# Performance work log

Hardware: AMD Instinct MI355X
Metric: run time of the kernel (lower is better)

The kernel has to match this reference:

```python
import jax, jax.numpy as jnp
import numpy as np

N = 8192
DIM_IN = 256
DIM_Q = 64
DIM_K = 64
E = 262144


def setup_inputs() -> dict:
    key = jax.random.key(0)
    ks = jax.random.split(key, 8)
    x = jax.random.normal(ks[0], (N, DIM_IN), dtype=jnp.float32)
    edge_index = jax.random.randint(ks[1], (2, E), 0, N, dtype=jnp.int64)
    s_in = 1.0 / np.sqrt(DIM_IN)
    Wq = jax.random.normal(ks[2], (DIM_IN, DIM_Q), dtype=jnp.float32) * s_in
    bq = jnp.zeros((DIM_Q,), dtype=jnp.float32)
    Wk = jax.random.normal(ks[3], (DIM_IN, DIM_K), dtype=jnp.float32) * s_in
    bk = jnp.zeros((DIM_K,), dtype=jnp.float32)
    Wv = jax.random.normal(ks[4], (DIM_IN, DIM_K), dtype=jnp.float32) * s_in
    bv = jnp.zeros((DIM_K,), dtype=jnp.float32)
    return {"x": x, "edge_index": edge_index, "Wq": Wq, "bq": bq,
            "Wk": Wk, "bk": bk, "Wv": Wv, "bv": bv}


def reference(x, edge_index, Wq, bq, Wk, bk, Wv, bv):
    # q/k/v projections (Dense layers)
    q = x @ Wq + bq            # (N, dim_q)
    k = x @ Wk + bk            # (N, dim_k)
    v = x @ Wv + bv            # (N, dim_k)
    n = x.shape[0]
    # scatter-built dense adjacency, as in the original module
    adj = jnp.zeros((n, n), dtype=x.dtype).at[edge_index[0], edge_index[1]].set(1.0)
    scale = 1.0 / jnp.sqrt(jnp.asarray(q.shape[-1], dtype=x.dtype))
    a = (q @ k.T) * scale      # (N, N)
    a = a * adj + (1.0 - adj) * (-1000000.0)
    attn = jax.nn.softmax(a, axis=-1)
    return attn @ v            # (N, dim_k)
```

## Files before the change

### kernel.cpp

```cpp
#include <hip/hip_runtime.h>
#include <hip/hip_bf16.h>

#define NROW 8192
#define DIM_IN 256
#define DIMK 64
#define NDIM 192
#define NEDGE 262144
#define BUCKET 128

using bf16 = __hip_bfloat16;
typedef _Float16 f16;
typedef _Float16 f16x8 __attribute__((ext_vector_type(8)));
typedef _Float16 f16x4 __attribute__((ext_vector_type(4)));
typedef float f32x4 __attribute__((ext_vector_type(4)));

__device__ __forceinline__ float b2f(bf16 x) { return __bfloat162float(x); }
__device__ __forceinline__ float us2f(unsigned short u) {
    return __uint_as_float(((unsigned)u) << 16);
}
__device__ __forceinline__ void wave_sync() {
    asm volatile("s_waitcnt lgkmcnt(0)" ::: "memory");
    __builtin_amdgcn_sched_barrier(0);
}

__global__ __launch_bounds__(256) void probe_kernel(
    const unsigned short* __restrict__ xw, const int* __restrict__ ei,
    int* __restrict__ cursor, int* __restrict__ eflag, int* __restrict__ fflag)
{
    int gid = blockIdx.x * 256 + threadIdx.x;
    cursor[gid] = 0;
    if (blockIdx.x == 0) {
        __shared__ int cnt, ebad;
        int t = threadIdx.x;
        if (t == 0) { cnt = 0; ebad = 0; }
        __syncthreads();
        if (t < 128) {
            int ex = (xw[t] >> 7) & 0xFF;
            if (ex >= 100 && ex <= 140) atomicAdd(&cnt, 1);
            if (t < 64 && ei[2 * t + 1] != 0) atomicAdd(&ebad, 1);
        }
        __syncthreads();
        if (t == 0) {
            *fflag = (cnt >= 110) ? 1 : 0;
            *eflag = (ebad == 0) ? 1 : 0;
        }
    }
}

__device__ __forceinline__ int src_at(const int* p, int e, int is64) {
    return is64 ? p[2 * e] : p[e];
}
__device__ __forceinline__ int dst_at(const int* p, int e, int is64) {
    return is64 ? p[2 * (NEDGE + e)] : p[NEDGE + e];
}

__global__ __launch_bounds__(256) void prep_kernel(
    const void* __restrict__ x,
    const void* __restrict__ Wq, const void* __restrict__ Wk,
    const void* __restrict__ Wv, const int* __restrict__ fflag,
    f16* __restrict__ xh, f16* __restrict__ wt)
{
    int isb = *fflag;
    int i = blockIdx.x * 256 + threadIdx.x;
    f16x4 o;
    if (isb) {
        ushort4 u = ((const ushort4*)x)[i];
        o.x = (f16)us2f(u.x); o.y = (f16)us2f(u.y);
        o.z = (f16)us2f(u.z); o.w = (f16)us2f(u.w);
    } else {
        float4 f = ((const float4*)x)[i];
        o.x = (f16)f.x; o.y = (f16)f.y; o.z = (f16)f.z; o.w = (f16)f.w;
    }
    *(f16x4*)(xh + 4 * i) = o;

    if (blockIdx.x < NDIM) {
        int d = blockIdx.x, c = threadIdx.x;
        int mat = d >> 6, dd = d & 63;
        const void* W = (mat == 0) ? Wq : (mat == 1) ? Wk : Wv;
        float val = isb ? b2f(((const bf16*)W)[c * DIMK + dd])
                        : ((const float*)W)[c * DIMK + dd];
        wt[d * DIM_IN + c] = (f16)val;
    }
}

__global__ __launch_bounds__(512) void proj_mfma_kernel(
    const f16* __restrict__ xh, const f16* __restrict__ wt,
    const void* __restrict__ bq, const void* __restrict__ bk,
    const void* __restrict__ bv, const int* __restrict__ fflag,
    f16* __restrict__ q, f16* __restrict__ k, f16* __restrict__ v)
{
    int t = threadIdx.x;
    int wave = t >> 6, lane = t & 63;
    int rowg = wave >> 2, colg = wave & 3;
    int r0 = blockIdx.x * 32 + rowg * 16;
    int n0 = colg * 48;
    int lr = lane & 15;
    int lk = (lane >> 4) * 8;

    f32x4 acc0 = {0.f, 0.f, 0.f, 0.f}, acc1 = acc0, acc2 = acc0;
    const f16* ap = xh + (size_t)(r0 + lr) * DIM_IN + lk;
    const f16* bp = wt + (size_t)(n0 + lr) * DIM_IN + lk;

    #pragma unroll
    for (int ks = 0; ks < 8; ++ks) {
        f16x8 a  = *(const f16x8*)(ap + ks * 32);
        f16x8 b0 = *(const f16x8*)(bp + ks * 32);
        f16x8 b1 = *(const f16x8*)(bp + 16 * DIM_IN + ks * 32);
        f16x8 b2 = *(const f16x8*)(bp + 32 * DIM_IN + ks * 32);
        acc0 = __builtin_amdgcn_mfma_f32_16x16x32_f16(a, b0, acc0, 0, 0, 0);
        acc1 = __builtin_amdgcn_mfma_f32_16x16x32_f16(a, b1, acc1, 0, 0, 0);
        acc2 = __builtin_amdgcn_mfma_f32_16x16x32_f16(a, b2, acc2, 0, 0, 0);
    }

    int isb = *fflag;
    #pragma unroll
    for (int tt = 0; tt < 3; ++tt) {
        f32x4 a = (tt == 0) ? acc0 : (tt == 1) ? acc1 : acc2;
        int d = n0 + tt * 16 + lr;
        int mat = d >> 6, dd = d & 63;
        const void* bb = (mat == 0) ? bq : (mat == 1) ? bk : bv;
        float bias = isb ? b2f(((const bf16*)bb)[dd]) : ((const float*)bb)[dd];
        f16* o = (mat == 0) ? q : (mat == 1) ? k : v;
        #pragma unroll
        for (int j = 0; j < 4; ++j) {
            int r = r0 + (lane >> 4) * 4 + j;
            o[(size_t)r * DIMK + dd] = (f16)(a[j] + bias);
        }
    }
}

__global__ __launch_bounds__(256) void scatter_kernel(
    const int* __restrict__ p, const int* __restrict__ eflag,
    int* __restrict__ cursor, unsigned short* __restrict__ colsbuf)
{
    int e = blockIdx.x * 256 + threadIdx.x;
    int is64 = *eflag;
    int r = src_at(p, e, is64);
    int c = dst_at(p, e, is64);
    int pos = atomicAdd(&cursor[r], 1);
    if (pos < BUCKET) colsbuf[(size_t)r * BUCKET + pos] = (unsigned short)c;
}

__global__ __launch_bounds__(256) void attn_kernel(
    const f16* __restrict__ q, const f16* __restrict__ k,
    const f16* __restrict__ v, const int* __restrict__ cursor,
    const unsigned short* __restrict__ colsbuf, float* __restrict__ out)
{
    __shared__ unsigned bm_all[4][NROW / 32];
    __shared__ unsigned short nb_all[4][BUCKET];
    __shared__ float sc_all[4][BUCKET];

    int t = threadIdx.x, wave = t >> 6, lane = t & 63;
    int row = blockIdx.x * 4 + wave;
    unsigned* bm = bm_all[wave];
    unsigned short* nb = nb_all[wave];
    float* sc = sc_all[wave];

    *(uint4*)(bm + 4 * lane) = make_uint4(0u, 0u, 0u, 0u);
    wave_sync();

    int deg = cursor[row];
    if (deg > BUCKET) deg = BUCKET;
    const unsigned short* bucket = colsbuf + (size_t)row * BUCKET;
    for (int e = lane; e < deg; e += 64) {
        int j = bucket[e];
        atomicOr(&bm[j >> 5], 1u << (j & 31));
    }
    wave_sync();

    uint4 wv = *(const uint4*)(bm + 4 * lane);
    int pc = __popc(wv.x) + __popc(wv.y) + __popc(wv.z) + __popc(wv.w);
    int incl = pc;
    #pragma unroll
    for (int o = 1; o < 64; o <<= 1) {
        int n = __shfl_up(incl, o);
        if (lane >= o) incl += n;
    }
    int nn = __shfl(incl, 63);
    int idx = incl - pc;
    unsigned wrds[4] = {wv.x, wv.y, wv.z, wv.w};
    #pragma unroll
    for (int wi = 0; wi < 4; ++wi) {
        unsigned wb = wrds[wi];
        int boff = 128 * lane + 32 * wi;
        while (wb) {
            int b = __ffs(wb) - 1;
            wb &= wb - 1;
            nb[idx++] = (unsigned short)(boff + b);
        }
    }
    wave_sync();

    if (nn == 0) {
        out[(size_t)row * DIMK + lane] = 0.f;
        return;
    }

    int g = lane >> 4, gl = lane & 15;
    f16x4 qh4 = *(const f16x4*)(q + (size_t)row * DIMK + 4 * gl);
    float q0 = (float)qh4.x, q1 = (float)qh4.y, q2 = (float)qh4.z, q3 = (float)qh4.w;
    for (int i = g; i < nn; i += 4) {
        int j = nb[i];
        f16x4 kk = *(const f16x4*)(k + (size_t)j * DIMK + 4 * gl);
        float d = q0 * (float)kk.x + q1 * (float)kk.y
                + q2 * (float)kk.z + q3 * (float)kk.w;
        #pragma unroll
        for (int o = 1; o < 16; o <<= 1) d += __shfl_xor(d, o);
        if (gl == 0) sc[i] = d * 0.125f;
    }
    wave_sync();

    float s0 = (lane < nn) ? sc[lane] : -INFINITY;
    float s1 = (lane + 64 < nn) ? sc[lane + 64] : -INFINITY;
    float mx = fmaxf(s0, s1);
    #pragma unroll
    for (int o = 1; o < 64; o <<= 1) mx = fmaxf(mx, __shfl_xor(mx, o));
    float w0 = (lane < nn) ? __expf(s0 - mx) : 0.f;
    float w1 = (lane + 64 < nn) ? __expf(s1 - mx) : 0.f;
    if (lane < nn) sc[lane] = w0;
    if (lane + 64 < nn) sc[lane + 64] = w1;
    float sm = w0 + w1;
    #pragma unroll
    for (int o = 1; o < 64; o <<= 1) sm += __shfl_xor(sm, o);
    wave_sync();

    float acc = 0.f;
    int i = 0;
    for (; i + 4 <= nn; i += 4) {
        int j0 = nb[i], j1 = nb[i + 1], j2 = nb[i + 2], j3 = nb[i + 3];
        float v0 = (float)v[(size_t)j0 * DIMK + lane];
        float v1 = (float)v[(size_t)j1 * DIMK + lane];
        float v2 = (float)v[(size_t)j2 * DIMK + lane];
        float v3 = (float)v[(size_t)j3 * DIMK + lane];
        acc = fmaf(sc[i], v0, acc);
        acc = fmaf(sc[i + 1], v1, acc);
        acc = fmaf(sc[i + 2], v2, acc);
        acc = fmaf(sc[i + 3], v3, acc);
    }
    for (; i < nn; ++i)
        acc = fmaf(sc[i], (float)v[(size_t)nb[i] * DIMK + lane], acc);

    out[(size_t)row * DIMK + lane] = acc / sm;
}

extern "C" void kernel_launch(void* const* d_in, const int* in_sizes, int n_in,
                              void* d_out, int out_size, void* d_ws, size_t ws_size,
                              hipStream_t stream)
{
    const void* x  = d_in[0];
    const int*  ei = (const int*)d_in[1];
    const void* Wq = d_in[2];
    const void* bq = d_in[3];
    const void* Wk = d_in[4];
    const void* bk = d_in[5];
    const void* Wv = d_in[6];
    const void* bv = d_in[7];
    float* out = (float*)d_out;

    char* W8 = (char*)d_ws;
    f16* xh = (f16*)W8;
    unsigned short* colsbuf = (unsigned short*)W8;
    f16* wt = (f16*)(W8 + (size_t)4 * 1024 * 1024);
    f16* qh = (f16*)(W8 + (size_t)4 * 1024 * 1024 + 98304);
    f16* kh = qh + (size_t)NROW * DIMK;
    f16* vh = kh + (size_t)NROW * DIMK;
    int* cursor = (int*)(vh + (size_t)NROW * DIMK);
    int* eflag = cursor + NROW;
    int* fflag = eflag + 1;
    size_t need = (size_t)((char*)(fflag + 1) - W8);
    if (ws_size < need) return;

    probe_kernel<<<32, 256, 0, stream>>>((const unsigned short*)x, ei,
                                         cursor, eflag, fflag);
    prep_kernel<<<2048, 256, 0, stream>>>(x, Wq, Wk, Wv, fflag, xh, wt);
    proj_mfma_kernel<<<NROW / 32, 512, 0, stream>>>(xh, wt, bq, bk, bv, fflag,
                                                    qh, kh, vh);
    scatter_kernel<<<NEDGE / 256, 256, 0, stream>>>(ei, eflag, cursor, colsbuf);
    attn_kernel<<<NROW / 4, 256, 0, stream>>>(qh, kh, vh, cursor, colsbuf, out);
}
```

Baseline: 52.67 us.

## Build global adjacency bitmap in projection kernel, drop probe and scatter kernels

```diff
diff --git a/kernel.cpp b/kernel.cpp
--- a/kernel.cpp
+++ b/kernel.cpp
@@ -6,7 +6,8 @@
 #define DIMK 64
 #define NDIM 192
 #define NEDGE 262144
-#define BUCKET 128
+#define NBW (NROW / 32)
+#define CAP 128
 
 using bf16 = __hip_bfloat16;
 typedef _Float16 f16;
@@ -23,30 +24,15 @@
     __builtin_amdgcn_sched_barrier(0);
 }
 
-__global__ __launch_bounds__(256) void probe_kernel(
-    const unsigned short* __restrict__ xw, const int* __restrict__ ei,
-    int* __restrict__ cursor, int* __restrict__ eflag, int* __restrict__ fflag)
-{
-    int gid = blockIdx.x * 256 + threadIdx.x;
-    cursor[gid] = 0;
-    if (blockIdx.x == 0) {
-        __shared__ int cnt, ebad;
-        int t = threadIdx.x;
-        if (t == 0) { cnt = 0; ebad = 0; }
-        __syncthreads();
-        if (t < 128) {
-            int ex = (xw[t] >> 7) & 0xFF;
-            if (ex >= 100 && ex <= 140) atomicAdd(&cnt, 1);
-            if (t < 64 && ei[2 * t + 1] != 0) atomicAdd(&ebad, 1);
-        }
-        __syncthreads();
-        if (t == 0) {
-            *fflag = (cnt >= 110) ? 1 : 0;
-            *eflag = (ebad == 0) ? 1 : 0;
-        }
-    }
-}
-
+__device__ __forceinline__ int probe_isb(const unsigned short* xw, int lane) {
+    int ex = (xw[lane] >> 7) & 0xFF;
+    unsigned long long b = __ballot(ex >= 100 && ex <= 140);
+    return (__popcll(b) >= 56) ? 1 : 0;
+}
+__device__ __forceinline__ int probe_is64(const int* ei, int lane) {
+    unsigned long long b = __ballot(ei[2 * lane + 1] != 0);
+    return (b == 0ULL) ? 1 : 0;
+}
 __device__ __forceinline__ int src_at(const int* p, int e, int is64) {
     return is64 ? p[2 * e] : p[e];
 }
@@ -57,11 +43,15 @@
 __global__ __launch_bounds__(256) void prep_kernel(
     const void* __restrict__ x,
     const void* __restrict__ Wq, const void* __restrict__ Wk,
-    const void* __restrict__ Wv, const int* __restrict__ fflag,
-    f16* __restrict__ xh, f16* __restrict__ wt)
-{
-    int isb = *fflag;
-    int i = blockIdx.x * 256 + threadIdx.x;
+    const void* __restrict__ Wv,
+    f16* __restrict__ xh, f16* __restrict__ wt, unsigned* __restrict__ gbm)
+{
+    int t = threadIdx.x, lane = t & 63;
+    int isb = probe_isb((const unsigned short*)x, lane);
+    int i = blockIdx.x * 256 + t;
+
+    ((uint4*)gbm)[i] = make_uint4(0u, 0u, 0u, 0u);
+
     f16x4 o;
     if (isb) {
         ushort4 u = ((const ushort4*)x)[i];
@@ -74,7 +64,7 @@
     *(f16x4*)(xh + 4 * i) = o;
 
     if (blockIdx.x < NDIM) {
-        int d = blockIdx.x, c = threadIdx.x;
+        int d = blockIdx.x, c = t;
         int mat = d >> 6, dd = d & 63;
         const void* W = (mat == 0) ? Wq : (mat == 1) ? Wk : Wv;
         float val = isb ? b2f(((const bf16*)W)[c * DIMK + dd])
@@ -83,14 +73,26 @@
     }
 }
 
-__global__ __launch_bounds__(512) void proj_mfma_kernel(
+__global__ __launch_bounds__(512) void proj_scatter_kernel(
     const f16* __restrict__ xh, const f16* __restrict__ wt,
     const void* __restrict__ bq, const void* __restrict__ bk,
-    const void* __restrict__ bv, const int* __restrict__ fflag,
+    const void* __restrict__ bv,
+    const unsigned short* __restrict__ xw, const int* __restrict__ ei,
+    unsigned* __restrict__ gbm,
     f16* __restrict__ q, f16* __restrict__ k, f16* __restrict__ v)
 {
     int t = threadIdx.x;
     int wave = t >> 6, lane = t & 63;
+
+    int is64 = probe_is64(ei, lane);
+    #pragma unroll
+    for (int ii = 0; ii < 2; ++ii) {
+        int e = blockIdx.x * 1024 + t + ii * 512;
+        int r = src_at(ei, e, is64) & (NROW - 1);
+        int c = dst_at(ei, e, is64) & (NROW - 1);
+        atomicOr(&gbm[r * NBW + (c >> 5)], 1u << (c & 31));
+    }
+
     int rowg = wave >> 2, colg = wave & 3;
     int r0 = blockIdx.x * 32 + rowg * 16;
     int n0 = colg * 48;
@@ -112,7 +114,7 @@
         acc2 = __builtin_amdgcn_mfma_f32_16x16x32_f16(a, b2, acc2, 0, 0, 0);
     }
 
-    int isb = *fflag;
+    int isb = probe_isb(xw, lane);
     #pragma unroll
     for (int tt = 0; tt < 3; ++tt) {
         f32x4 a = (tt == 0) ? acc0 : (tt == 1) ? acc1 : acc2;
@@ -129,46 +131,20 @@
     }
 }
 
-__global__ __launch_bounds__(256) void scatter_kernel(
-    const int* __restrict__ p, const int* __restrict__ eflag,
-    int* __restrict__ cursor, unsigned short* __restrict__ colsbuf)
-{
-    int e = blockIdx.x * 256 + threadIdx.x;
-    int is64 = *eflag;
-    int r = src_at(p, e, is64);
-    int c = dst_at(p, e, is64);
-    int pos = atomicAdd(&cursor[r], 1);
-    if (pos < BUCKET) colsbuf[(size_t)r * BUCKET + pos] = (unsigned short)c;
-}
-
 __global__ __launch_bounds__(256) void attn_kernel(
     const f16* __restrict__ q, const f16* __restrict__ k,
-    const f16* __restrict__ v, const int* __restrict__ cursor,
-    const unsigned short* __restrict__ colsbuf, float* __restrict__ out)
-{
-    __shared__ unsigned bm_all[4][NROW / 32];
-    __shared__ unsigned short nb_all[4][BUCKET];
-    __shared__ float sc_all[4][BUCKET];
+    const f16* __restrict__ v, const unsigned* __restrict__ gbm,
+    float* __restrict__ out)
+{
+    __shared__ unsigned short nb_all[4][CAP];
+    __shared__ float sc_all[4][CAP];
 
     int t = threadIdx.x, wave = t >> 6, lane = t & 63;
     int row = blockIdx.x * 4 + wave;
-    unsigned* bm = bm_all[wave];
     unsigned short* nb = nb_all[wave];
     float* sc = sc_all[wave];
 
-    *(uint4*)(bm + 4 * lane) = make_uint4(0u, 0u, 0u, 0u);
-    wave_sync();
-
-    int deg = cursor[row];
-    if (deg > BUCKET) deg = BUCKET;
-    const unsigned short* bucket = colsbuf + (size_t)row * BUCKET;
-    for (int e = lane; e < deg; e += 64) {
-        int j = bucket[e];
-        atomicOr(&bm[j >> 5], 1u << (j & 31));
-    }
-    wave_sync();
-
-    uint4 wv = *(const uint4*)(bm + 4 * lane);
+    uint4 wv = *(const uint4*)(gbm + (size_t)row * NBW + 4 * lane);
     int pc = __popc(wv.x) + __popc(wv.y) + __popc(wv.z) + __popc(wv.w);
     int incl = pc;
     #pragma unroll
@@ -177,6 +153,7 @@
         if (lane >= o) incl += n;
     }
     int nn = __shfl(incl, 63);
+    if (nn > CAP) nn = CAP;
     int idx = incl - pc;
     unsigned wrds[4] = {wv.x, wv.y, wv.z, wv.w};
     #pragma unroll
@@ -186,7 +163,8 @@
         while (wb) {
             int b = __ffs(wb) - 1;
             wb &= wb - 1;
-            nb[idx++] = (unsigned short)(boff + b);
+            if (idx < CAP) nb[idx] = (unsigned short)(boff + b);
+            idx++;
         }
     }
     wave_sync();
@@ -259,22 +237,17 @@
 
     char* W8 = (char*)d_ws;
     f16* xh = (f16*)W8;
-    unsigned short* colsbuf = (unsigned short*)W8;
-    f16* wt = (f16*)(W8 + (size_t)4 * 1024 * 1024);
-    f16* qh = (f16*)(W8 + (size_t)4 * 1024 * 1024 + 98304);
+    unsigned* gbm = (unsigned*)(W8 + (size_t)4 * 1024 * 1024);
+    f16* wt = (f16*)(W8 + (size_t)12 * 1024 * 1024);
+    f16* qh = (f16*)(W8 + (size_t)12 * 1024 * 1024 + 98304);
     f16* kh = qh + (size_t)NROW * DIMK;
     f16* vh = kh + (size_t)NROW * DIMK;
-    int* cursor = (int*)(vh + (size_t)NROW * DIMK);
-    int* eflag = cursor + NROW;
-    int* fflag = eflag + 1;
-    size_t need = (size_t)((char*)(fflag + 1) - W8);
+    size_t need = (size_t)((char*)(vh + (size_t)NROW * DIMK) - W8);
     if (ws_size < need) return;
 
-    probe_kernel<<<32, 256, 0, stream>>>((const unsigned short*)x, ei,
-                                         cursor, eflag, fflag);
-    prep_kernel<<<2048, 256, 0, stream>>>(x, Wq, Wk, Wv, fflag, xh, wt);
-    proj_mfma_kernel<<<NROW / 32, 512, 0, stream>>>(xh, wt, bq, bk, bv, fflag,
-                                                    qh, kh, vh);
-    scatter_kernel<<<NEDGE / 256, 256, 0, stream>>>(ei, eflag, cursor, colsbuf);
-    attn_kernel<<<NROW / 4, 256, 0, stream>>>(qh, kh, vh, cursor, colsbuf, out);
-}
+    prep_kernel<<<2048, 256, 0, stream>>>(x, Wq, Wk, Wv, xh, wt, gbm);
+    proj_scatter_kernel<<<256, 512, 0, stream>>>(xh, wt, bq, bk, bv,
+                                                 (const unsigned short*)x, ei,
+                                                 gbm, qh, kh, vh);
+    attn_kernel<<<NROW / 4, 256, 0, stream>>>(qh, kh, vh, gbm, out);
+}
```

New measurement: 45.00 us, median of 2. -14.6%, faster.
